# Performance work log

Measured on AMD Instinct MI355X. Metric: run time of the kernel, lower is better.

Reference implementation:

```python
import jax, jax.numpy as jnp
import numpy as np

HID = 1024
HEADS = 16
DH = HID // HEADS
SCALE = DH ** -0.5
L, B = 2048, 2


def setup_inputs() -> dict:
    key = jax.random.key(0)
    ks = jax.random.split(key, 16)
    inp = {
        "query": jax.random.normal(ks[0], (L, B, HID), jnp.float32),
        "key": jax.random.normal(ks[1], (L, B, HID), jnp.float32),
        "value": jax.random.normal(ks[2], (L, B, HID), jnp.float32),
        "mask": jax.random.randint(ks[3], (B, L), 0, 2).astype(bool),
    }
    # xavier-uniform linear weights (torch Linear stores [out, in]; y = x @ W.T + b)
    lim = (6.0 / (HID + HID)) ** 0.5
    for i, name in enumerate(["wq", "wk", "wv", "wfc"]):
        inp[name] = jax.random.uniform(ks[4 + i], (HID, HID), jnp.float32, -lim, lim)
    inp["bq"] = jnp.zeros((HID,), jnp.float32)
    inp["bk"] = jnp.zeros((HID,), jnp.float32)
    inp["bv"] = jnp.zeros((HID,), jnp.float32)
    inp["bfc"] = jnp.zeros((HID,), jnp.float32)
    inp["tao"] = jnp.full((HEADS,), 10.0, jnp.float32)
    return inp


def reference(query, key, value, mask, wq, bq, wk, bk, wv, bv, wfc, bfc, tao):
    # inputs arrive [L, B, D]; module transposes to [B, L, D]
    q = jnp.swapaxes(query, 0, 1)
    k = jnp.swapaxes(key, 0, 1)
    v = jnp.swapaxes(value, 0, 1)
    bsz, length, _ = q.shape

    def heads(x, w, b):
        y = x @ w.T + b                      # [B, L, D]
        return y.reshape(bsz, length, HEADS, DH).transpose(0, 2, 1, 3)  # [B, H, L, d]

    Q = heads(q, wq, bq)
    K = heads(k, wk, bk)
    V = heads(v, wv, bv)

    qk = jnp.einsum("bhqd,bhkd->bhqk", Q, K) * SCALE  # [B, H, L, L]

    # gaussian positional bias: -|i-j|^2/2 * tao_h^-4
    idx = jnp.arange(length, dtype=jnp.float32)
    dist = -0.5 * (idx[:, None] - idx[None, :]) ** 2          # [L, L]
    qk = qk + dist[None, None, :, :] * (tao ** -4)[None, :, None, None]

    qk = jnp.where(mask[:, None, None, :], -jnp.inf, qk)
    attn = jax.nn.softmax(qk, axis=-1)  # dropout is identity in eval mode

    x = jnp.einsum("bhqk,bhkd->bhqd", attn, V)            # [B, H, L, d]
    x = x.transpose(0, 2, 1, 3).reshape(bsz, length, HID)  # [B, L, D]
    x = x @ wfc.T + bfc
    return jnp.swapaxes(x, 0, 1)  # [L, B, D]
```

## Files before the change

kernel.cpp:

```cpp
#include <hip/hip_runtime.h>

#define LQ   2048
#define BQ   2
#define HID  1024
#define NH   16
#define DH   64
#define SCALE 0.125f
#define L2E  1.44269504088896f
#define C1   0.18033688011f
#define EXPOFF 23.0831206542f

using short8  = __attribute__((ext_vector_type(8))) short;
using ushort8 = __attribute__((ext_vector_type(8))) unsigned short;
using f32x4   = __attribute__((ext_vector_type(4))) float;
typedef unsigned short u16;
typedef __attribute__((ext_vector_type(2))) __bf16 bf16x2;

__device__ inline u16 f2bf(float x) {
    unsigned int u = __float_as_uint(x);
    u = (u + 0x7fffu + ((u >> 16) & 1u)) >> 16;
    return (u16)u;
}

#if defined(__has_builtin)
#if __has_builtin(__builtin_amdgcn_cvt_pk_bf16_f32)
#define HAVE_PKBF 1
#endif
#if __has_builtin(__builtin_amdgcn_exp2f)
#define HAVE_EXP2 1
#endif
#endif

__device__ inline unsigned int pkbf(float a, float b) {
#ifdef HAVE_PKBF
    bf16x2 r = __builtin_amdgcn_cvt_pk_bf16_f32(a, b);
    return __builtin_bit_cast(unsigned int, r);
#else
    return (unsigned int)f2bf(a) | ((unsigned int)f2bf(b) << 16);
#endif
}

__device__ inline float fexp2(float x) {
#ifdef HAVE_EXP2
    return __builtin_amdgcn_exp2f(x);
#else
    return exp2f(x);
#endif
}

__device__ inline void gl_lds16(const void* g, void* l) {
    __builtin_amdgcn_global_load_lds(
        (const __attribute__((address_space(1))) void*)g,
        (__attribute__((address_space(3))) void*)l, 16, 0, 0);
}

struct CastArgs {
    const float* s[7];
    u16* d[7];
    int n[7];
    const unsigned char* mraw;
    int* mout;
    int mn;
};

__global__ __launch_bounds__(256) void castw(CastArgs a) {
    const int y = blockIdx.y;
    const int t = threadIdx.x;
    if (y == 7) {
        if (blockIdx.x != 0) return;
        __shared__ int cnt;
        if (t == 0) cnt = 0;
        __syncthreads();
        int local = 0;
        for (int i = t; i < a.mn; i += 256)
            if ((i & 3) && a.mraw[i]) local++;
        atomicAdd(&cnt, local);
        __syncthreads();
        bool isInt32 = (cnt == 0);
        const int* mi = (const int*)a.mraw;
        for (int i = t; i < a.mn; i += 256)
            a.mout[i] = isInt32 ? mi[i] : (int)a.mraw[i];
        return;
    }
    const float* s = a.s[y];
    u16* d = a.d[y];
    const int n4 = a.n[y] >> 2;
    for (int i = blockIdx.x * 256 + t; i < n4; i += gridDim.x * 256) {
        float4 v = *(const float4*)(s + (size_t)i * 4);
        uint2 p;
        p.x = pkbf(v.x, v.y);
        p.y = pkbf(v.z, v.w);
        *(uint2*)(d + (size_t)i * 4) = p;
    }
}

struct QkvArgs {
    const u16* A[3];
    const u16* W[3];
    const float* bias[3];
    u16* out[3];
};

__global__ __launch_bounds__(256) void gemm_qkv(QkvArgs ga) {
    __shared__ u16 As[2][128][64];
    __shared__ u16 Bs[2][128][64];

    const int z = blockIdx.z;
    const u16* A = ga.A[z];
    const u16* W = ga.W[z];
    const float* bias = ga.bias[z];
    u16* outp = ga.out[z];

    const int t = threadIdx.x;
    const int m0 = blockIdx.x * 128;
    const int n0 = blockIdx.y * 128;
    const int lane = t & 63;
    const int lane15 = lane & 15;
    const int quad = lane >> 4;
    const int w = t >> 6;
    const int wm = (w >> 1) * 64;
    const int wn = (w & 1) * 64;

    const int lrow = lane >> 3;
    const int ch = (lane & 7) ^ ((lane >> 3) & 7);
    const u16* aS = A + (size_t)(m0 + 32 * w + lrow) * HID + 8 * ch;
    const u16* bS = W + (size_t)(n0 + 32 * w + lrow) * HID + 8 * ch;

    const int s0 = (quad ^ (lane15 & 7)) * 8;
    const int s1 = ((4 + quad) ^ (lane15 & 7)) * 8;

    f32x4 acc[4][4];
#pragma unroll
    for (int i = 0; i < 4; i++)
#pragma unroll
        for (int j = 0; j < 4; j++) acc[i][j] = (f32x4){0,0,0,0};

#pragma unroll
    for (int i = 0; i < 4; i++) {
        gl_lds16(aS + (size_t)(8 * i) * HID, &As[0][32 * w + 8 * i][0]);
        gl_lds16(bS + (size_t)(8 * i) * HID, &Bs[0][32 * w + 8 * i][0]);
    }
    __syncthreads();

    int p = 0;
    for (int k0 = 0; k0 < HID; k0 += 64) {
        short8 af0[4], af1[4], bf0[4], bf1[4];
#pragma unroll
        for (int i = 0; i < 4; i++) {
            const u16* ar = &As[p][wm + i * 16 + lane15][0];
            const u16* br = &Bs[p][wn + i * 16 + lane15][0];
            af0[i] = *(const short8*)(ar + s0);
            af1[i] = *(const short8*)(ar + s1);
            bf0[i] = *(const short8*)(br + s0);
            bf1[i] = *(const short8*)(br + s1);
        }
        if (k0 + 64 < HID) {
#pragma unroll
            for (int i = 0; i < 4; i++) {
                gl_lds16(aS + (size_t)(8 * i) * HID + (k0 + 64), &As[p ^ 1][32 * w + 8 * i][0]);
                gl_lds16(bS + (size_t)(8 * i) * HID + (k0 + 64), &Bs[p ^ 1][32 * w + 8 * i][0]);
            }
        }
#pragma unroll
        for (int mi = 0; mi < 4; mi++)
#pragma unroll
            for (int ni = 0; ni < 4; ni++) {
                acc[mi][ni] = __builtin_amdgcn_mfma_f32_16x16x32_bf16(af0[mi], bf0[ni], acc[mi][ni], 0, 0, 0);
                acc[mi][ni] = __builtin_amdgcn_mfma_f32_16x16x32_bf16(af1[mi], bf1[ni], acc[mi][ni], 0, 0, 0);
            }
        __syncthreads();
        p ^= 1;
    }

#pragma unroll
    for (int mi = 0; mi < 4; mi++) {
#pragma unroll
        for (int ni = 0; ni < 4; ni++) {
            const int n = n0 + wn + ni * 16 + lane15;
            const float bv = bias[n];
            const int h = n >> 6, d = n & 63;
#pragma unroll
            for (int r = 0; r < 4; r++) {
                const int m = m0 + wm + mi * 16 + quad * 4 + r;
                const float c = acc[mi][ni][r] + bv;
                const int b = m & 1, l = m >> 1;
                if (z < 2) {
                    outp[(((size_t)(b * NH + h)) * LQ + l) * DH + d] = f2bf(c);
                } else {
                    outp[(((size_t)(b * NH + h)) * DH + d) * LQ + l] = f2bf(c);
                }
            }
        }
    }
}

__global__ __launch_bounds__(256) void gemm_fc(const u16* __restrict__ A,
                                               const u16* __restrict__ W,
                                               const float* __restrict__ bias,
                                               float* __restrict__ outp) {
    __shared__ u16 As[2][128][64];
    __shared__ u16 Bs[2][64][64];

    const int t = threadIdx.x;
    const int m0 = blockIdx.x * 128;
    const int n0 = blockIdx.y * 64;
    const int lane = t & 63;
    const int lane15 = lane & 15;
    const int quad = lane >> 4;
    const int w = t >> 6;
    const int wm = (w >> 1) * 64;
    const int wn = (w & 1) * 32;

    const int lrow = lane >> 3;
    const int ch = (lane & 7) ^ ((lane >> 3) & 7);
    const u16* aS = A + (size_t)(m0 + 32 * w + lrow) * HID + 8 * ch;
    const u16* bS = W + (size_t)(n0 + 16 * w + lrow) * HID + 8 * ch;

    const int s0 = (quad ^ (lane15 & 7)) * 8;
    const int s1 = ((4 + quad) ^ (lane15 & 7)) * 8;

    f32x4 acc[4][2];
#pragma unroll
    for (int i = 0; i < 4; i++)
#pragma unroll
        for (int j = 0; j < 2; j++) acc[i][j] = (f32x4){0,0,0,0};

#pragma unroll
    for (int i = 0; i < 4; i++)
        gl_lds16(aS + (size_t)(8 * i) * HID, &As[0][32 * w + 8 * i][0]);
#pragma unroll
    for (int i = 0; i < 2; i++)
        gl_lds16(bS + (size_t)(8 * i) * HID, &Bs[0][16 * w + 8 * i][0]);
    __syncthreads();

    int p = 0;
    for (int k0 = 0; k0 < HID; k0 += 64) {
        short8 af0[4], af1[4], bf0[2], bf1[2];
#pragma unroll
        for (int i = 0; i < 4; i++) {
            const u16* ar = &As[p][wm + i * 16 + lane15][0];
            af0[i] = *(const short8*)(ar + s0);
            af1[i] = *(const short8*)(ar + s1);
        }
#pragma unroll
        for (int j = 0; j < 2; j++) {
            const u16* br = &Bs[p][wn + j * 16 + lane15][0];
            bf0[j] = *(const short8*)(br + s0);
            bf1[j] = *(const short8*)(br + s1);
        }
        if (k0 + 64 < HID) {
#pragma unroll
            for (int i = 0; i < 4; i++)
                gl_lds16(aS + (size_t)(8 * i) * HID + (k0 + 64), &As[p ^ 1][32 * w + 8 * i][0]);
#pragma unroll
            for (int i = 0; i < 2; i++)
                gl_lds16(bS + (size_t)(8 * i) * HID + (k0 + 64), &Bs[p ^ 1][16 * w + 8 * i][0]);
        }
#pragma unroll
        for (int mi = 0; mi < 4; mi++)
#pragma unroll
            for (int ni = 0; ni < 2; ni++) {
                acc[mi][ni] = __builtin_amdgcn_mfma_f32_16x16x32_bf16(af0[mi], bf0[ni], acc[mi][ni], 0, 0, 0);
                acc[mi][ni] = __builtin_amdgcn_mfma_f32_16x16x32_bf16(af1[mi], bf1[ni], acc[mi][ni], 0, 0, 0);
            }
        __syncthreads();
        p ^= 1;
    }

#pragma unroll
    for (int mi = 0; mi < 4; mi++) {
#pragma unroll
        for (int ni = 0; ni < 2; ni++) {
            const int n = n0 + wn + ni * 16 + lane15;
            const float bv = bias[n];
#pragma unroll
            for (int r = 0; r < 4; r++) {
                const int m = m0 + wm + mi * 16 + quad * 4 + r;
                outp[(size_t)m * HID + n] = acc[mi][ni][r] + bv;
            }
        }
    }
}

#define PSTR 72

__global__ __launch_bounds__(512) void attn_kernel(const u16* __restrict__ Qg,
                                                   const u16* __restrict__ Kg,
                                                   const u16* __restrict__ Vtg,
                                                   const int* __restrict__ maskI,
                                                   const float* __restrict__ tao,
                                                   u16* __restrict__ Xa) {
    __shared__ u16 Ks[2][64][64];
    __shared__ u16 Vt[2][64][64];
    __shared__ u16 PT[128][PSTR];
    __shared__ float smaskF[LQ];

    const int bh = blockIdx.x;
    const int q0 = blockIdx.y * 128;
    const int b = bh >> 4;
    const int h = bh & 15;
    const int t = threadIdx.x;
    const int w = t >> 6;
    const int lane = t & 63;
    const int lane15 = lane & 15;
    const int quad = lane >> 4;

    const u16* Kbase = Kg + (size_t)bh * LQ * DH;
    const u16* Vtbase = Vtg + (size_t)bh * DH * LQ;
    const int* mrow = maskI + b * LQ;

    const float tv = tao[h];
    const float t2 = tv * tv;
    const float nb = -0.5f / (t2 * t2);
    const float nb2 = nb * L2E;
    const float sqn = sqrtf(-nb2);
    const float R = sqrtf(-40.0f / nb2) + 1.0f;

    int c_lo = (int)floorf(((float)q0 - R) * (1.0f / 64.0f));
    int c_hi = (int)floorf(((float)(q0 + 127) + R) * (1.0f / 64.0f));
    if (c_lo < 0) c_lo = 0;
    if (c_hi > (LQ / 64 - 1)) c_hi = LQ / 64 - 1;
    if (c_hi < c_lo) c_hi = c_lo;

    const int lr = lane >> 3;
    const int lc = lane & 7;
    const int sch = lc ^ lr;
    const u16* kS = Kbase + (size_t)(8 * w + lr) * DH + 8 * sch;
    const u16* vS = Vtbase + (size_t)(8 * w + lr) * LQ + 8 * sch;

    gl_lds16(kS + (size_t)(64 * c_lo) * DH, &Ks[0][8 * w][0]);
    gl_lds16(vS + 64 * c_lo, &Vt[0][8 * w][0]);
    for (int i = t; i < LQ; i += 512)
        smaskF[i] = mrow[i] ? -3.0e38f : -EXPOFF;

    const int qrow = q0 + w * 16 + lane15;
    short8 qB0, qB1;
    {
        const u16* qp_ = Qg + ((size_t)bh * LQ + qrow) * DH + quad * 8;
        qB0 = *(const short8*)(qp_);
        qB1 = *(const short8*)(qp_ + 32);
    }

    const int s0 = (quad ^ (lane15 & 7)) * 8;
    const int s1 = ((4 + quad) ^ (lane15 & 7)) * 8;

    f32x4 O[4];
#pragma unroll
    for (int mt = 0; mt < 4; mt++) O[mt] = (f32x4){0,0,0,0};
    float l_ = 0.0f;

    const float ebase0 = (float)(qrow - quad * 4);
    const int prow = w * 16 + lane15;

    __syncthreads();

    int p = 0;
    for (int c = c_lo; c <= c_hi; ++c) {
        if (c < c_hi) {
            gl_lds16(kS + (size_t)(64 * (c + 1)) * DH, &Ks[p ^ 1][8 * w][0]);
            gl_lds16(vS + 64 * (c + 1), &Vt[p ^ 1][8 * w][0]);
        }

        f32x4 S[4];
#pragma unroll
        for (int kt = 0; kt < 4; kt++) {
            const u16* kr = &Ks[p][kt * 16 + lane15][0];
            const short8 ka = *(const short8*)(kr + s0);
            const short8 kb = *(const short8*)(kr + s1);
            S[kt] = __builtin_amdgcn_mfma_f32_16x16x32_bf16(ka, qB0, (f32x4){0,0,0,0}, 0, 0, 0);
            S[kt] = __builtin_amdgcn_mfma_f32_16x16x32_bf16(kb, qB1, S[kt], 0, 0, 0);
        }

        const float eb = (ebase0 - (float)(64 * c)) * sqn;
        float lacc = 0.0f;
#pragma unroll
        for (int kt = 0; kt < 4; kt++) {
            const float4 sm4 = *(const float4*)&smaskF[64 * c + kt * 16 + quad * 4];
            float pr[4];
#pragma unroll
            for (int r = 0; r < 4; r++) {
                const float dp = eb - (float)(kt * 16 + r) * sqn;
                const float tb = fmaf(-dp, dp, ((const float*)&sm4)[r]);
                pr[r] = fexp2(fmaf(S[kt][r], C1, tb));
                lacc += pr[r];
            }
            uint2 pk2;
            pk2.x = pkbf(pr[0], pr[1]);
            pk2.y = pkbf(pr[2], pr[3]);
            *(uint2*)&PT[prow][kt * 16 + quad * 4] = pk2;
        }
        l_ += lacc;

        const short8 pB0 = *(const short8*)&PT[prow][quad * 8];
        const short8 pB1 = *(const short8*)&PT[prow][32 + quad * 8];
#pragma unroll
        for (int mt = 0; mt < 4; mt++) {
            const u16* vr = &Vt[p][mt * 16 + lane15][0];
            const short8 va = *(const short8*)(vr + s0);
            const short8 vb = *(const short8*)(vr + s1);
            O[mt] = __builtin_amdgcn_mfma_f32_16x16x32_bf16(va, pB0, O[mt], 0, 0, 0);
            O[mt] = __builtin_amdgcn_mfma_f32_16x16x32_bf16(vb, pB1, O[mt], 0, 0, 0);
        }

        __syncthreads();
        p ^= 1;
    }

    l_ += __shfl_xor(l_, 16, 64);
    l_ += __shfl_xor(l_, 32, 64);

    {
        const float inv = 1.0f / l_;
        u16* dst = Xa + ((size_t)qrow * BQ + b) * HID + h * DH;
#pragma unroll
        for (int mt = 0; mt < 4; mt++) {
            uint2 pk2;
            pk2.x = pkbf(O[mt][0] * inv, O[mt][1] * inv);
            pk2.y = pkbf(O[mt][2] * inv, O[mt][3] * inv);
            *(uint2*)(dst + mt * 16 + quad * 4) = pk2;
        }
    }
}

extern "C" void kernel_launch(void* const* d_in, const int* in_sizes, int n_in,
                              void* d_out, int out_size, void* d_ws, size_t ws_size,
                              hipStream_t stream) {
    const float* q    = (const float*)d_in[0];
    const float* k    = (const float*)d_in[1];
    const float* v    = (const float*)d_in[2];
    const void*  mask = d_in[3];
    const float* wq   = (const float*)d_in[4];
    const float* wk   = (const float*)d_in[5];
    const float* wv   = (const float*)d_in[6];
    const float* wfc  = (const float*)d_in[7];
    const float* bq   = (const float*)d_in[8];
    const float* bk   = (const float*)d_in[9];
    const float* bv   = (const float*)d_in[10];
    const float* bfc  = (const float*)d_in[11];
    const float* tao  = (const float*)d_in[12];

    const size_t NE = (size_t)LQ * BQ * HID;
    const size_t NW = (size_t)HID * HID;
    u16* base = (u16*)d_ws;
    u16* Qp    = base;
    u16* Kp    = base + NE;
    u16* Vtp   = base + 2 * NE;
    u16* Xa    = base + 3 * NE;
    u16* qbf   = base + 4 * NE;
    u16* kbf   = base + 5 * NE;
    u16* vbf   = base + 6 * NE;
    u16* wqbf  = base + 7 * NE;
    u16* wkbf  = wqbf + NW;
    u16* wvbf  = wkbf + NW;
    u16* wfcbf = wvbf + NW;
    int* maskI = (int*)(wfcbf + NW);

    CastArgs ca;
    ca.s[0] = q;   ca.d[0] = qbf;   ca.n[0] = (int)NE;
    ca.s[1] = k;   ca.d[1] = kbf;   ca.n[1] = (int)NE;
    ca.s[2] = v;   ca.d[2] = vbf;   ca.n[2] = (int)NE;
    ca.s[3] = wq;  ca.d[3] = wqbf;  ca.n[3] = (int)NW;
    ca.s[4] = wk;  ca.d[4] = wkbf;  ca.n[4] = (int)NW;
    ca.s[5] = wv;  ca.d[5] = wvbf;  ca.n[5] = (int)NW;
    ca.s[6] = wfc; ca.d[6] = wfcbf; ca.n[6] = (int)NW;
    ca.mraw = (const unsigned char*)mask;
    ca.mout = maskI;
    ca.mn = BQ * LQ;
    castw<<<dim3(256, 8), 256, 0, stream>>>(ca);

    QkvArgs ga;
    ga.A[0] = qbf;  ga.W[0] = wqbf;  ga.bias[0] = bq;  ga.out[0] = Qp;
    ga.A[1] = kbf;  ga.W[1] = wkbf;  ga.bias[1] = bk;  ga.out[1] = Kp;
    ga.A[2] = vbf;  ga.W[2] = wvbf;  ga.bias[2] = bv;  ga.out[2] = Vtp;
    gemm_qkv<<<dim3(32, 8, 3), 256, 0, stream>>>(ga);

    attn_kernel<<<dim3(32, 16), 512, 0, stream>>>(Qp, Kp, Vtp, maskI, tao, Xa);

    gemm_fc<<<dim3(32, 16), 256, 0, stream>>>(Xa, wfcbf, bfc, (float*)d_out);
}
```

Baseline: 240.8 us.

## Shrink attention blocks to 64 queries and move row-sum into MFMA

The attention kernel now uses 256-thread blocks covering 64 query rows (grid doubled to 32x32), and each wave loads two K/V rows per chunk. The softmax denominator is computed with an MFMA against a ones vector instead of per-lane adds and shuffles. The mask is precomputed as float bias in the cast kernel and read from global per chunk, replacing the per-block 2048-entry LDS mask fill. Per-column distance offsets are precomputed into registers. Smaller blocks narrow the band of key chunks each block visits and add blocks for occupancy, at the cost of reloading K/V across more blocks and extra MFMA work for the sums. The masked bias changes from -3e38 to -1024 offset, which is treated as effectively zero after exp2.

After: 236.5 us. No clear change (-1.8%).

```diff
diff --git a/kernel.cpp b/kernel.cpp
--- a/kernel.cpp
+++ b/kernel.cpp
@@ -9,6 +9,7 @@
 #define L2E  1.44269504088896f
 #define C1   0.18033688011f
 #define EXPOFF 23.0831206542f
+#define MASKNEG (-1024.0f)
 
 using short8  = __attribute__((ext_vector_type(8))) short;
 using ushort8 = __attribute__((ext_vector_type(8))) unsigned short;
@@ -59,7 +60,7 @@
     u16* d[7];
     int n[7];
     const unsigned char* mraw;
-    int* mout;
+    float* mout;
     int mn;
 };
 
@@ -78,8 +79,10 @@
         __syncthreads();
         bool isInt32 = (cnt == 0);
         const int* mi = (const int*)a.mraw;
-        for (int i = t; i < a.mn; i += 256)
-            a.mout[i] = isInt32 ? mi[i] : (int)a.mraw[i];
+        for (int i = t; i < a.mn; i += 256) {
+            const bool m = isInt32 ? (mi[i] != 0) : (a.mraw[i] != 0);
+            a.mout[i] = m ? (MASKNEG - EXPOFF) : (-EXPOFF);
+        }
         return;
     }
     const float* s = a.s[y];
@@ -284,19 +287,18 @@
 
 #define PSTR 72
 
-__global__ __launch_bounds__(512) void attn_kernel(const u16* __restrict__ Qg,
-                                                   const u16* __restrict__ Kg,
-                                                   const u16* __restrict__ Vtg,
-                                                   const int* __restrict__ maskI,
-                                                   const float* __restrict__ tao,
-                                                   u16* __restrict__ Xa) {
+__global__ __launch_bounds__(256, 3) void attn_kernel(const u16* __restrict__ Qg,
+                                                      const u16* __restrict__ Kg,
+                                                      const u16* __restrict__ Vtg,
+                                                      const float* __restrict__ maskF,
+                                                      const float* __restrict__ tao,
+                                                      u16* __restrict__ Xa) {
     __shared__ u16 Ks[2][64][64];
     __shared__ u16 Vt[2][64][64];
-    __shared__ u16 PT[128][PSTR];
-    __shared__ float smaskF[LQ];
+    __shared__ u16 PT[64][PSTR];
 
     const int bh = blockIdx.x;
-    const int q0 = blockIdx.y * 128;
+    const int q0 = blockIdx.y * 64;
     const int b = bh >> 4;
     const int h = bh & 15;
     const int t = threadIdx.x;
@@ -307,7 +309,7 @@
 
     const u16* Kbase = Kg + (size_t)bh * LQ * DH;
     const u16* Vtbase = Vtg + (size_t)bh * DH * LQ;
-    const int* mrow = maskI + b * LQ;
+    const float* mrow = maskF + b * LQ;
 
     const float tv = tao[h];
     const float t2 = tv * tv;
@@ -317,21 +319,17 @@
     const float R = sqrtf(-40.0f / nb2) + 1.0f;
 
     int c_lo = (int)floorf(((float)q0 - R) * (1.0f / 64.0f));
-    int c_hi = (int)floorf(((float)(q0 + 127) + R) * (1.0f / 64.0f));
+    int c_hi = (int)floorf(((float)(q0 + 63) + R) * (1.0f / 64.0f));
     if (c_lo < 0) c_lo = 0;
     if (c_hi > (LQ / 64 - 1)) c_hi = LQ / 64 - 1;
     if (c_hi < c_lo) c_hi = c_lo;
 
     const int lr = lane >> 3;
-    const int lc = lane & 7;
-    const int sch = lc ^ lr;
-    const u16* kS = Kbase + (size_t)(8 * w + lr) * DH + 8 * sch;
-    const u16* vS = Vtbase + (size_t)(8 * w + lr) * LQ + 8 * sch;
-
-    gl_lds16(kS + (size_t)(64 * c_lo) * DH, &Ks[0][8 * w][0]);
-    gl_lds16(vS + 64 * c_lo, &Vt[0][8 * w][0]);
-    for (int i = t; i < LQ; i += 512)
-        smaskF[i] = mrow[i] ? -3.0e38f : -EXPOFF;
+    const int sch = (lane & 7) ^ lr;
+    const u16* kS0 = Kbase + (size_t)(16 * w + lr) * DH + 8 * sch;
+    const u16* kS1 = Kbase + (size_t)(16 * w + 8 + lr) * DH + 8 * sch;
+    const u16* vS0 = Vtbase + (size_t)(16 * w + lr) * LQ + 8 * sch;
+    const u16* vS1 = Vtbase + (size_t)(16 * w + 8 + lr) * LQ + 8 * sch;
 
     const int qrow = q0 + w * 16 + lane15;
     short8 qB0, qB1;
@@ -344,21 +342,41 @@
     const int s0 = (quad ^ (lane15 & 7)) * 8;
     const int s1 = ((4 + quad) ^ (lane15 & 7)) * 8;
 
+    float crs[16];
+#pragma unroll
+    for (int i = 0; i < 16; i++)
+        crs[i] = (float)((i >> 2) * 16 + (i & 3)) * sqn;
+
+    short8 ones;
+#pragma unroll
+    for (int i = 0; i < 8; i++) ones[i] = (short)0x3F80;
+
     f32x4 O[4];
 #pragma unroll
     for (int mt = 0; mt < 4; mt++) O[mt] = (f32x4){0,0,0,0};
-    float l_ = 0.0f;
-
-    const float ebase0 = (float)(qrow - quad * 4);
+    f32x4 Lacc = (f32x4){0,0,0,0};
+
+    const float eb0 = (float)(qrow - quad * 4);
     const int prow = w * 16 + lane15;
 
+    gl_lds16(kS0 + (size_t)c_lo * (64 * DH), &Ks[0][16 * w][0]);
+    gl_lds16(kS1 + (size_t)c_lo * (64 * DH), &Ks[0][16 * w + 8][0]);
+    gl_lds16(vS0 + 64 * c_lo, &Vt[0][16 * w][0]);
+    gl_lds16(vS1 + 64 * c_lo, &Vt[0][16 * w + 8][0]);
     __syncthreads();
 
     int p = 0;
     for (int c = c_lo; c <= c_hi; ++c) {
+        float4 mv[4];
+#pragma unroll
+        for (int kt = 0; kt < 4; kt++)
+            mv[kt] = *(const float4*)(mrow + 64 * c + kt * 16 + quad * 4);
+
         if (c < c_hi) {
-            gl_lds16(kS + (size_t)(64 * (c + 1)) * DH, &Ks[p ^ 1][8 * w][0]);
-            gl_lds16(vS + 64 * (c + 1), &Vt[p ^ 1][8 * w][0]);
+            gl_lds16(kS0 + (size_t)(c + 1) * (64 * DH), &Ks[p ^ 1][16 * w][0]);
+            gl_lds16(kS1 + (size_t)(c + 1) * (64 * DH), &Ks[p ^ 1][16 * w + 8][0]);
+            gl_lds16(vS0 + 64 * (c + 1), &Vt[p ^ 1][16 * w][0]);
+            gl_lds16(vS1 + 64 * (c + 1), &Vt[p ^ 1][16 * w + 8][0]);
         }
 
         f32x4 S[4];
@@ -371,28 +389,28 @@
             S[kt] = __builtin_amdgcn_mfma_f32_16x16x32_bf16(kb, qB1, S[kt], 0, 0, 0);
         }
 
-        const float eb = (ebase0 - (float)(64 * c)) * sqn;
-        float lacc = 0.0f;
+        const float ebS = (eb0 - (float)(64 * c)) * sqn;
+        float lacc_dummy;
+        (void)lacc_dummy;
 #pragma unroll
         for (int kt = 0; kt < 4; kt++) {
-            const float4 sm4 = *(const float4*)&smaskF[64 * c + kt * 16 + quad * 4];
             float pr[4];
 #pragma unroll
             for (int r = 0; r < 4; r++) {
-                const float dp = eb - (float)(kt * 16 + r) * sqn;
-                const float tb = fmaf(-dp, dp, ((const float*)&sm4)[r]);
+                const float dp = ebS - crs[kt * 4 + r];
+                const float tb = fmaf(-dp, dp, ((const float*)&mv[kt])[r]);
                 pr[r] = fexp2(fmaf(S[kt][r], C1, tb));
-                lacc += pr[r];
             }
             uint2 pk2;
             pk2.x = pkbf(pr[0], pr[1]);
             pk2.y = pkbf(pr[2], pr[3]);
             *(uint2*)&PT[prow][kt * 16 + quad * 4] = pk2;
         }
-        l_ += lacc;
 
         const short8 pB0 = *(const short8*)&PT[prow][quad * 8];
         const short8 pB1 = *(const short8*)&PT[prow][32 + quad * 8];
+        Lacc = __builtin_amdgcn_mfma_f32_16x16x32_bf16(ones, pB0, Lacc, 0, 0, 0);
+        Lacc = __builtin_amdgcn_mfma_f32_16x16x32_bf16(ones, pB1, Lacc, 0, 0, 0);
 #pragma unroll
         for (int mt = 0; mt < 4; mt++) {
             const u16* vr = &Vt[p][mt * 16 + lane15][0];
@@ -406,11 +424,8 @@
         p ^= 1;
     }
 
-    l_ += __shfl_xor(l_, 16, 64);
-    l_ += __shfl_xor(l_, 32, 64);
-
     {
-        const float inv = 1.0f / l_;
+        const float inv = 1.0f / Lacc[0];
         u16* dst = Xa + ((size_t)qrow * BQ + b) * HID + h * DH;
 #pragma unroll
         for (int mt = 0; mt < 4; mt++) {
@@ -453,7 +468,7 @@
     u16* wkbf  = wqbf + NW;
     u16* wvbf  = wkbf + NW;
     u16* wfcbf = wvbf + NW;
-    int* maskI = (int*)(wfcbf + NW);
+    float* maskF = (float*)(wfcbf + NW);
 
     CastArgs ca;
     ca.s[0] = q;   ca.d[0] = qbf;   ca.n[0] = (int)NE;
@@ -464,7 +479,7 @@
     ca.s[5] = wv;  ca.d[5] = wvbf;  ca.n[5] = (int)NW;
     ca.s[6] = wfc; ca.d[6] = wfcbf; ca.n[6] = (int)NW;
     ca.mraw = (const unsigned char*)mask;
-    ca.mout = maskI;
+    ca.mout = maskF;
     ca.mn = BQ * LQ;
     castw<<<dim3(256, 8), 256, 0, stream>>>(ca);
 
@@ -474,7 +489,7 @@
     ga.A[2] = vbf;  ga.W[2] = wvbf;  ga.bias[2] = bv;  ga.out[2] = Vtp;
     gemm_qkv<<<dim3(32, 8, 3), 256, 0, stream>>>(ga);
 
-    attn_kernel<<<dim3(32, 16), 512, 0, stream>>>(Qp, Kp, Vtp, maskI, tao, Xa);
+    attn_kernel<<<dim3(32, 32), 256, 0, stream>>>(Qp, Kp, Vtp, maskF, tao, Xa);
 
     gemm_fc<<<dim3(32, 16), 256, 0, stream>>>(Xa, wfcbf, bfc, (float*)d_out);
 }
```
